# Performance work log

Measured on AMD Instinct MI355X. Metric: run time of the kernel, lower is better.

Reference implementation:

```python
import jax, jax.numpy as jnp
import numpy as np


def setup_inputs() -> dict:
    key = jax.random.key(0)
    k1, k2 = jax.random.split(key)
    B, N, M, D = 4, 8192, 8192, 3
    input1 = jax.random.normal(k1, (B, N, D), dtype=jnp.float32)
    input2 = jax.random.normal(k2, (B, M, D), dtype=jnp.float32)
    return {"input1": input1, "input2": input2}


def reference(input1, input2):
    x2 = jnp.sum(input1 * input1, axis=-1)              # [B, N]
    y2 = jnp.sum(input2 * input2, axis=-1)              # [B, M]
    xy = jnp.einsum('bnd,bmd->bnm', input1, input2)     # [B, N, M]
    d2 = x2[:, :, None] + y2[:, None, :] - 2.0 * xy     # [B, N, M]
    d2 = jnp.maximum(d2, 0.0)
    dist1 = jnp.min(d2, axis=2)  # [B, N] nearest in input2 for each point in input1
    dist2 = jnp.min(d2, axis=1)  # [B, M] nearest in input1 for each point in input2
    # Chamfer loss: mean of both directional terms
    return jnp.mean(dist1) + jnp.mean(dist2)
```

## Files before the change

kernel.cpp:

```cpp
#include <hip/hip_runtime.h>

#define NB     4
#define NPTS   8192
#define NTP    (NPTS / 2)
#define TPB    512
#define QPC    32
#define NCHUNK 4
#define SLOTS  64
#define ITERS  (NTP / TPB)

typedef float v4f __attribute__((ext_vector_type(4)));

__device__ __forceinline__ unsigned fkey(float f) {
    int b = __float_as_int(f);
    return (unsigned)(b ^ ((b >> 31) | 0x80000000));
}
__device__ __forceinline__ float funkey(unsigned k) {
    int b = (k & 0x80000000u) ? (int)(k ^ 0x80000000u) : ~(int)k;
    return __int_as_float(b);
}

__global__ void pack_pts(const float* __restrict__ in1, const float* __restrict__ in2,
                         v4f* __restrict__ nq, v4f* __restrict__ tp) {
    int i = blockIdx.x * blockDim.x + threadIdx.x;
    if (i < NB * NPTS) {
        float x = in1[3*i], y = in1[3*i+1], z = in1[3*i+2];
        nq[i] = (v4f){x, y, z, 0.5f * (x*x + y*y + z*z)};
    } else {
        int p = i - NB * NPTS;
        float x0 = in2[6*p+0], y0 = in2[6*p+1], z0 = in2[6*p+2];
        float x1 = in2[6*p+3], y1 = in2[6*p+4], z1 = in2[6*p+5];
        tp[2*p]   = (v4f){x0, x1, y0, y1};
        tp[2*p+1] = (v4f){z0, z1, 0.5f*(x0*x0 + y0*y0 + z0*z0),
                                  0.5f*(x1*x1 + y1*y1 + z1*z1)};
    }
}

__launch_bounds__(TPB, 1)
__global__ void chamfer_min(const v4f* __restrict__ nq, const v4f* __restrict__ tp,
                            unsigned* __restrict__ colbuf, float* __restrict__ accum) {
    __shared__ unsigned colkey[NPTS];
    __shared__ float red[8][QPC];

    const int slot = blockIdx.x;
    const int bb   = blockIdx.y;
    const int t    = threadIdx.x;
    const int lane = t & 63;
    const int wave = t >> 6;

    uint4 ff = make_uint4(~0u, ~0u, ~0u, ~0u);
#pragma unroll
    for (int k = 0; k < 4; ++k) ((uint4*)colkey)[t + k * TPB] = ff;
    __syncthreads();

    const v4f* __restrict__ Tb = tp + (size_t)bb * (2 * NTP);
    const v4f* __restrict__ Qb = nq + (size_t)bb * NPTS + slot * (NCHUNK * QPC);

    for (int chunk = 0; chunk < NCHUNK; ++chunk) {
        float qx[QPC], qy[QPC], qz[QPC], qw[QPC];
#pragma unroll
        for (int j = 0; j < QPC; ++j) {
            v4f q = Qb[chunk * QPC + j];
            qx[j] = q.x; qy[j] = q.y; qz[j] = q.z; qw[j] = q.w;
            asm("" : "+v"(qx[j]), "+v"(qy[j]), "+v"(qz[j]), "+v"(qw[j]));
        }

        float accR[QPC];
#pragma unroll
        for (int j = 0; j < QPC; ++j) accR[j] = 1e30f;

        int idx = t;
        v4f tl = Tb[2 * idx], th = Tb[2 * idx + 1];

#pragma unroll 1
        for (int it = 0; it < ITERS; ++it) {
            int nidx = (idx + TPB) & (NTP - 1);
            v4f ntl = Tb[2 * nidx], nth = Tb[2 * nidx + 1];

            float x0 = tl.x, x1 = tl.y, y0 = tl.z, y1 = tl.w;
            float z0 = th.x, z1 = th.y, w0 = th.z, w1 = th.w;
            float c0 = 1e30f, c1 = 1e30f;
#pragma unroll
            for (int j = 0; j < QPC; j += 2) {
                float f0 = fmaf(-qx[j],   x0, fmaf(-qy[j],   y0, fmaf(-qz[j],   z0, w0 + qw[j])));
                float f1 = fmaf(-qx[j],   x1, fmaf(-qy[j],   y1, fmaf(-qz[j],   z1, w1 + qw[j])));
                float g0 = fmaf(-qx[j+1], x0, fmaf(-qy[j+1], y0, fmaf(-qz[j+1], z0, w0 + qw[j+1])));
                float g1 = fmaf(-qx[j+1], x1, fmaf(-qy[j+1], y1, fmaf(-qz[j+1], z1, w1 + qw[j+1])));
                asm("v_min3_f32 %0, %0, %1, %2" : "+v"(accR[j])   : "v"(f0), "v"(f1));
                asm("v_min3_f32 %0, %0, %1, %2" : "+v"(accR[j+1]) : "v"(g0), "v"(g1));
                asm("v_min3_f32 %0, %0, %1, %2" : "+v"(c0)        : "v"(f0), "v"(g0));
                asm("v_min3_f32 %0, %0, %1, %2" : "+v"(c1)        : "v"(f1), "v"(g1));
            }
            atomicMin(&colkey[idx],       fkey(c0));
            atomicMin(&colkey[NTP + idx], fkey(c1));
            tl = ntl; th = nth; idx = nidx;
        }

#pragma unroll
        for (int j = 0; j < QPC; ++j) {
            float a = accR[j];
            a = fminf(a, __shfl_xor(a, 32));
            a = fminf(a, __shfl_xor(a, 16));
            a = fminf(a, __shfl_xor(a, 8));
            a = fminf(a, __shfl_xor(a, 4));
            a = fminf(a, __shfl_xor(a, 2));
            a = fminf(a, __shfl_xor(a, 1));
            accR[j] = a;
        }
        if (lane == 0) {
#pragma unroll
            for (int j = 0; j < QPC; j += 4)
                *(v4f*)&red[wave][j] = (v4f){accR[j], accR[j+1], accR[j+2], accR[j+3]};
        }
        __syncthreads();
        if (t < QPC) {
            float m = red[0][t];
#pragma unroll
            for (int w = 1; w < 8; ++w) m = fminf(m, red[w][t]);
            float dist = fmaxf(2.0f * m, 0.0f);
#pragma unroll
            for (int off = 16; off > 0; off >>= 1)
                dist += __shfl_xor(dist, off, 32);
            if (t == 0) atomicAdd(accum, dist);
        }
        __syncthreads();
    }

    uint4* cb = (uint4*)(colbuf + (size_t)(bb * SLOTS + slot) * NPTS);
#pragma unroll
    for (int k = 0; k < 4; ++k) cb[t + k * TPB] = ((uint4*)colkey)[t + k * TPB];
}

__global__ void col_combine(const unsigned* __restrict__ colbuf, float* __restrict__ accum) {
    int tid = blockIdx.x * blockDim.x + threadIdx.x;
    int bb  = tid >> 11;
    int m4  = tid & 2047;
    const uint4* cb = (const uint4*)(colbuf + (size_t)bb * SLOTS * NPTS);
    uint4 k = make_uint4(~0u, ~0u, ~0u, ~0u);
#pragma unroll 4
    for (int s = 0; s < SLOTS; ++s) {
        uint4 v = cb[s * (NPTS / 4) + m4];
        k.x = min(k.x, v.x); k.y = min(k.y, v.y);
        k.z = min(k.z, v.z); k.w = min(k.w, v.w);
    }
    float dist = fmaxf(2.0f * funkey(k.x), 0.0f) + fmaxf(2.0f * funkey(k.y), 0.0f)
               + fmaxf(2.0f * funkey(k.z), 0.0f) + fmaxf(2.0f * funkey(k.w), 0.0f);
    for (int off = 32; off > 0; off >>= 1) dist += __shfl_xor(dist, off, 64);
    if ((threadIdx.x & 63) == 0) atomicAdd(accum, dist);
}

__global__ void finish(const float* __restrict__ accum, float* __restrict__ out) {
    out[0] = accum[0] * (1.0f / (NB * NPTS));
}

extern "C" void kernel_launch(void* const* d_in, const int* in_sizes, int n_in,
                              void* d_out, int out_size, void* d_ws, size_t ws_size,
                              hipStream_t stream) {
    const float* in1 = (const float*)d_in[0];
    const float* in2 = (const float*)d_in[1];

    char* ws = (char*)d_ws;
    float*    accum  = (float*)ws;
    v4f*      nq     = (v4f*)(ws + 256);
    v4f*      tp     = nq + (size_t)NB * NPTS;
    unsigned* colbuf = (unsigned*)(tp + (size_t)NB * NTP * 2);

    hipMemsetAsync(accum, 0, sizeof(float), stream);

    pack_pts<<<dim3((NB * NPTS + NB * NTP) / 256), 256, 0, stream>>>(in1, in2, nq, tp);

    chamfer_min<<<dim3(SLOTS, NB), TPB, 0, stream>>>(nq, tp, colbuf, accum);

    col_combine<<<dim3(32), 256, 0, stream>>>(colbuf, accum);

    finish<<<1, 1, 0, stream>>>(accum, (float*)d_out);
}
```

Measured before the change: 77.77 us.

## Shrink blocks and query chunks, raise slot count, simplify column min keys

Measured after the change: 74.42 us. -4.3%, faster.

```diff
diff --git a/kernel.cpp b/kernel.cpp
--- a/kernel.cpp
+++ b/kernel.cpp
@@ -3,22 +3,11 @@
 #define NB     4
 #define NPTS   8192
 #define NTP    (NPTS / 2)
-#define TPB    512
-#define QPC    32
-#define NCHUNK 4
-#define SLOTS  64
+#define TPB    256
+#define QPC    16
 #define ITERS  (NTP / TPB)
 
 typedef float v4f __attribute__((ext_vector_type(4)));
-
-__device__ __forceinline__ unsigned fkey(float f) {
-    int b = __float_as_int(f);
-    return (unsigned)(b ^ ((b >> 31) | 0x80000000));
-}
-__device__ __forceinline__ float funkey(unsigned k) {
-    int b = (k & 0x80000000u) ? (int)(k ^ 0x80000000u) : ~(int)k;
-    return __int_as_float(b);
-}
 
 __global__ void pack_pts(const float* __restrict__ in1, const float* __restrict__ in2,
                          v4f* __restrict__ nq, v4f* __restrict__ tp) {
@@ -36,11 +25,13 @@
     }
 }
 
-__launch_bounds__(TPB, 1)
+template<int SLOTS>
+__launch_bounds__(TPB, 4)
 __global__ void chamfer_min(const v4f* __restrict__ nq, const v4f* __restrict__ tp,
                             unsigned* __restrict__ colbuf, float* __restrict__ accum) {
+    constexpr int NCHUNK = (NPTS / SLOTS) / QPC;
     __shared__ unsigned colkey[NPTS];
-    __shared__ float red[8][QPC];
+    __shared__ float red[4][QPC];
 
     const int slot = blockIdx.x;
     const int bb   = blockIdx.y;
@@ -50,12 +41,13 @@
 
     uint4 ff = make_uint4(~0u, ~0u, ~0u, ~0u);
 #pragma unroll
-    for (int k = 0; k < 4; ++k) ((uint4*)colkey)[t + k * TPB] = ff;
+    for (int k = 0; k < NPTS / 4 / TPB; ++k) ((uint4*)colkey)[t + k * TPB] = ff;
     __syncthreads();
 
     const v4f* __restrict__ Tb = tp + (size_t)bb * (2 * NTP);
     const v4f* __restrict__ Qb = nq + (size_t)bb * NPTS + slot * (NCHUNK * QPC);
 
+#pragma unroll 1
     for (int chunk = 0; chunk < NCHUNK; ++chunk) {
         float qx[QPC], qy[QPC], qz[QPC], qw[QPC];
 #pragma unroll
@@ -91,8 +83,8 @@
                 asm("v_min3_f32 %0, %0, %1, %2" : "+v"(c0)        : "v"(f0), "v"(g0));
                 asm("v_min3_f32 %0, %0, %1, %2" : "+v"(c1)        : "v"(f1), "v"(g1));
             }
-            atomicMin(&colkey[idx],       fkey(c0));
-            atomicMin(&colkey[NTP + idx], fkey(c1));
+            atomicMin(&colkey[idx],       __float_as_uint(fmaxf(c0, 0.0f)));
+            atomicMin(&colkey[NTP + idx], __float_as_uint(fmaxf(c1, 0.0f)));
             tl = ntl; th = nth; idx = nidx;
         }
 
@@ -114,13 +106,11 @@
         }
         __syncthreads();
         if (t < QPC) {
-            float m = red[0][t];
-#pragma unroll
-            for (int w = 1; w < 8; ++w) m = fminf(m, red[w][t]);
+            float m = fminf(fminf(red[0][t], red[1][t]), fminf(red[2][t], red[3][t]));
             float dist = fmaxf(2.0f * m, 0.0f);
 #pragma unroll
-            for (int off = 16; off > 0; off >>= 1)
-                dist += __shfl_xor(dist, off, 32);
+            for (int off = 8; off > 0; off >>= 1)
+                dist += __shfl_xor(dist, off, 16);
             if (t == 0) atomicAdd(accum, dist);
         }
         __syncthreads();
@@ -128,23 +118,19 @@
 
     uint4* cb = (uint4*)(colbuf + (size_t)(bb * SLOTS + slot) * NPTS);
 #pragma unroll
-    for (int k = 0; k < 4; ++k) cb[t + k * TPB] = ((uint4*)colkey)[t + k * TPB];
+    for (int k = 0; k < NPTS / 4 / TPB; ++k) cb[t + k * TPB] = ((uint4*)colkey)[t + k * TPB];
 }
 
+template<int SLOTS>
 __global__ void col_combine(const unsigned* __restrict__ colbuf, float* __restrict__ accum) {
     int tid = blockIdx.x * blockDim.x + threadIdx.x;
-    int bb  = tid >> 11;
-    int m4  = tid & 2047;
-    const uint4* cb = (const uint4*)(colbuf + (size_t)bb * SLOTS * NPTS);
-    uint4 k = make_uint4(~0u, ~0u, ~0u, ~0u);
-#pragma unroll 4
-    for (int s = 0; s < SLOTS; ++s) {
-        uint4 v = cb[s * (NPTS / 4) + m4];
-        k.x = min(k.x, v.x); k.y = min(k.y, v.y);
-        k.z = min(k.z, v.z); k.w = min(k.w, v.w);
-    }
-    float dist = fmaxf(2.0f * funkey(k.x), 0.0f) + fmaxf(2.0f * funkey(k.y), 0.0f)
-               + fmaxf(2.0f * funkey(k.z), 0.0f) + fmaxf(2.0f * funkey(k.w), 0.0f);
+    int bb  = tid >> 13;
+    int m   = tid & (NPTS - 1);
+    const unsigned* cb = colbuf + (size_t)bb * SLOTS * NPTS + m;
+    unsigned k = ~0u;
+#pragma unroll 8
+    for (int s = 0; s < SLOTS; ++s) k = min(k, cb[(size_t)s * NPTS]);
+    float dist = 2.0f * __uint_as_float(k);
     for (int off = 32; off > 0; off >>= 1) dist += __shfl_xor(dist, off, 64);
     if ((threadIdx.x & 63) == 0) atomicAdd(accum, dist);
 }
@@ -166,12 +152,18 @@
     unsigned* colbuf = (unsigned*)(tp + (size_t)NB * NTP * 2);
 
     hipMemsetAsync(accum, 0, sizeof(float), stream);
-
     pack_pts<<<dim3((NB * NPTS + NB * NTP) / 256), 256, 0, stream>>>(in1, in2, nq, tp);
 
-    chamfer_min<<<dim3(SLOTS, NB), TPB, 0, stream>>>(nq, tp, colbuf, accum);
+    const size_t base = 256 + (size_t)NB * NPTS * 16 * 2;
+    const size_t need128 = base + (size_t)128 * NB * NPTS * 4;
 
-    col_combine<<<dim3(32), 256, 0, stream>>>(colbuf, accum);
+    if (ws_size >= need128) {
+        chamfer_min<128><<<dim3(128, NB), TPB, 0, stream>>>(nq, tp, colbuf, accum);
+        col_combine<128><<<dim3(128), 256, 0, stream>>>(colbuf, accum);
+    } else {
+        chamfer_min<64><<<dim3(64, NB), TPB, 0, stream>>>(nq, tp, colbuf, accum);
+        col_combine<64><<<dim3(128), 256, 0, stream>>>(colbuf, accum);
+    }
 
     finish<<<1, 1, 0, stream>>>(accum, (float*)d_out);
 }
```
